# Kernel optimization log

Hardware: AMD Instinct MI355X
Metric: run time of the kernel (lower is better)

## Reference

```python
import jax, jax.numpy as jnp
import numpy as np

B, NB, K, C, CM, POS = 8, 1024, 9, 32, 128, 2
SIGMA = 0.5
NEG_SLOPE = 0.01  # nn.LeakyReLU default
BN_EPS = 1e-5


def _leaky(x):
    return jnp.where(x >= 0, x, NEG_SLOPE * x)


def _batchnorm(x, gamma, beta):
    # BatchNorm1d, training-mode batch statistics over the point dimension
    mu = jnp.mean(x, axis=0)
    var = jnp.mean((x - mu) ** 2, axis=0)
    return gamma * (x - mu) * jax.lax.rsqrt(var + BN_EPS) + beta


def setup_inputs() -> dict:
    key = jax.random.key(0)
    ks = jax.random.split(key, 8)
    N = B * NB
    positions = jax.random.normal(ks[0], (N, POS), jnp.float32)
    weights = jax.random.normal(ks[1], (N, C), jnp.float32)
    batch = jnp.full((B,), NB, dtype=jnp.int32)  # uniform point counts per graph
    # KernelConv params: kernel_init='grid' -> 3x3 grid of offsets spanning +-sigma
    g = jnp.linspace(-SIGMA, SIGMA, 3, dtype=jnp.float32)
    kernel_positions = jnp.stack(jnp.meshgrid(g, g, indexing='ij'), axis=-1).reshape(K, POS)
    kernel_weights = (jax.random.normal(ks[2], (K, C, C), jnp.float32) / np.float32(np.sqrt(C * K)))
    conv_norm_gamma = jnp.ones((C,), jnp.float32)
    conv_norm_beta = jnp.zeros((C,), jnp.float32)
    # PyG MLP([C, CM, C+POS], act_first=True, plain_last=True)
    W1 = jax.random.normal(ks[3], (C, CM), jnp.float32) / np.float32(np.sqrt(C))
    b1 = jnp.zeros((CM,), jnp.float32)
    bn_gamma = jnp.ones((CM,), jnp.float32)
    bn_beta = jnp.zeros((CM,), jnp.float32)
    W2 = jax.random.normal(ks[4], (CM, C + POS), jnp.float32) / np.float32(np.sqrt(CM))
    b2 = jnp.zeros((C + POS,), jnp.float32)
    return dict(positions=positions, weights=weights, batch=batch,
                kernel_positions=kernel_positions, kernel_weights=kernel_weights,
                conv_norm_gamma=conv_norm_gamma, conv_norm_beta=conv_norm_beta,
                W1=W1, b1=b1, bn_gamma=bn_gamma, bn_beta=bn_beta, W2=W2, b2=b2)


def reference(positions, weights, batch, kernel_positions, kernel_weights,
              conv_norm_gamma, conv_norm_beta, W1, b1, bn_gamma, bn_beta, W2, b2):
    N = positions.shape[0]
    # --- KernelConv: each point spawns K components at pos + kernel offset ---
    conv_pos = (positions[:, None, :] + kernel_positions[None, :, :])  # [N,K,2]
    conv_w = jnp.einsum('nc,kcd->nkd', weights, kernel_weights)        # [N,K,C]
    conv_pos = conv_pos.reshape(B, NB * K, POS)
    conv_w = conv_w.reshape(B, NB * K, C)
    # --- KernelSample: evaluate Gaussian mixture at original positions ---
    p = positions.reshape(B, NB, POS)
    d2 = (jnp.sum(p * p, -1)[:, :, None]
          + jnp.sum(conv_pos * conv_pos, -1)[:, None, :]
          - 2.0 * jnp.einsum('bnd,bmd->bnm', p, conv_pos))             # [B,NB,NB*K]
    Kmat = jnp.exp(-d2 / (2.0 * SIGMA * SIGMA))
    sampled = jnp.einsum('bnm,bmc->bnc', Kmat, conv_w).reshape(N, C)
    x = _leaky(sampled)                                                 # KernelSample nonlinearity
    # conv_norm + residual add of input weights
    x = _batchnorm(x, conv_norm_gamma, conv_norm_beta) + weights
    # MLP: lin -> act -> batchnorm (act_first) -> plain last lin
    h = _batchnorm(_leaky(x @ W1 + b1), bn_gamma, bn_beta)
    mlp_out = h @ W2 + b2                                               # [N, POS + C]
    delta_pos, delta_w = mlp_out[:, :POS], mlp_out[:, POS:]
    return positions + delta_pos, x + delta_w
```

## Files before the change

kernel.cpp:

```cpp
#include <hip/hip_runtime.h>
#include <hip/hip_bf16.h>

#define BB    8
#define NBB   1024
#define KK    9
#define CC    32
#define CMM   128
#define NTOT  (BB*NBB)
#define MM    (NBB*KK)
#define MS    16
#define MR    (MM/MS)
#define NEG   0.01f
#define EPS   1e-5f
#define L2C   (-2.8853900817779268f)

#define OFF_CWT   0
#define SZ_CWT    (BB*CC*MM/2)
#define OFF_CFX   (OFF_CWT + SZ_CWT)
#define OFF_CFY   (OFF_CFX + BB*MM)
#define OFF_CF0   (OFF_CFY + BB*MM)
#define OFF_PART  (OFF_CF0 + BB*MM)
#define SZ_ONE    (NTOT*CC)
#define SZ_PART   (MS*SZ_ONE)
#define OFF_X0    (OFF_PART)
#define OFF_X     (OFF_PART + SZ_ONE)
#define OFF_H0    (OFF_PART + 2*SZ_ONE)
#define OFF_ST    (OFF_PART + SZ_PART)

typedef __attribute__((ext_vector_type(8))) short short8;
typedef __attribute__((ext_vector_type(4))) float f32x4;
typedef __attribute__((ext_vector_type(2))) float f32x2;

static __device__ __forceinline__ unsigned short f2bf_rne(float f) {
    __hip_bfloat16 h = __float2bfloat16(f);
    return *reinterpret_cast<unsigned short*>(&h);
}

__global__ __launch_bounds__(256) void k_prep(const float* __restrict__ pos,
                                              const float* __restrict__ kpos,
                                              float* __restrict__ cfx,
                                              float* __restrict__ cfy,
                                              float* __restrict__ cf0,
                                              float* __restrict__ stats) {
    int gid = blockIdx.x*256 + threadIdx.x;
    if (blockIdx.x == 0 && threadIdx.x < 320) stats[threadIdx.x] = 0.f;
    if (gid < BB*MM) {
        int b = gid / MM;
        int m = gid - b*MM;
        int np = m / 9, k9 = m - np*9;
        float qx = pos[((size_t)(b*NBB + np))*2 + 0] + kpos[k9*2 + 0];
        float qy = pos[((size_t)(b*NBB + np))*2 + 1] + kpos[k9*2 + 1];
        cfx[gid] = -2.f*L2C*qx;
        cfy[gid] = -2.f*L2C*qy;
        cf0[gid] = L2C*(qx*qx + qy*qy);
    }
}

__global__ __launch_bounds__(256) void k_convw(const float* __restrict__ w,
                                               const float* __restrict__ kw,
                                               short* __restrict__ cwT) {
    __shared__ unsigned short tile[4*32*144];
    int t = threadIdx.x;
    int l = t & 63, wv = t >> 6;
    int lane15 = l & 15, quad = l >> 4;
    int blk = blockIdx.x;
    int b = blk >> 4, nbl = blk & 15;
    int n = b*NBB + nbl*64 + wv*16 + lane15;

    f32x4 w0 = *(const f32x4*)&w[(size_t)n*CC + quad*8];
    f32x4 w1 = *(const f32x4*)&w[(size_t)n*CC + quad*8 + 4];
    union { unsigned short us[8]; short8 s; } bfr;
    bfr.us[0] = f2bf_rne(w0.x); bfr.us[1] = f2bf_rne(w0.y);
    bfr.us[2] = f2bf_rne(w0.z); bfr.us[3] = f2bf_rne(w0.w);
    bfr.us[4] = f2bf_rne(w1.x); bfr.us[5] = f2bf_rne(w1.y);
    bfr.us[6] = f2bf_rne(w1.z); bfr.us[7] = f2bf_rne(w1.w);

    f32x4 acc[KK][2];
    #pragma unroll
    for (int kk = 0; kk < KK; ++kk) {
        #pragma unroll
        for (int ct = 0; ct < 2; ++ct) {
            int c = ct*16 + lane15;
            union { unsigned short us[8]; short8 s; } afr;
            #pragma unroll
            for (int j = 0; j < 8; ++j)
                afr.us[j] = f2bf_rne(kw[(size_t)(kk*CC + quad*8 + j)*CC + c]);
            acc[kk][ct] = __builtin_amdgcn_mfma_f32_16x16x32_bf16(
                afr.s, bfr.s, (f32x4)0.f, 0, 0, 0);
        }
    }
    unsigned short* tw = tile + wv*4608;
    #pragma unroll
    for (int kk = 0; kk < KK; ++kk)
        #pragma unroll
        for (int ct = 0; ct < 2; ++ct)
            #pragma unroll
            for (int reg = 0; reg < 4; ++reg) {
                int c = ct*16 + quad*4 + reg;
                tw[c*144 + lane15*9 + kk] = f2bf_rne(acc[kk][ct][reg]);
            }
    __syncthreads();
    short* dst = cwT + (size_t)b*CC*MM + (size_t)(nbl*64 + wv*16)*9;
    #pragma unroll
    for (int it = 0; it < 9; ++it) {
        int u = it*64 + l;
        int c = u / 18, seg = u - c*18;
        short8 v = *(const short8*)&tw[c*144 + seg*8];
        *(short8*)&dst[(size_t)c*MM + seg*8] = v;
    }
}

__global__ __launch_bounds__(256) void k_sample(const float* __restrict__ pos,
                                                const float* __restrict__ cfx,
                                                const float* __restrict__ cfy,
                                                const float* __restrict__ cf0,
                                                const short* __restrict__ cwT,
                                                float* __restrict__ part) {
    int t = threadIdx.x;
    int l = t & 63, w = t >> 6;
    int blk = blockIdx.x;
    int ks = blk & 15, nb = (blk >> 4) & 7, b = blk >> 7;
    int lane15 = l & 15, quad = l >> 4;
    int nbase = b*NBB + nb*128 + w*32;

    float px[2], py[2], cn[2];
    #pragma unroll
    for (int nt = 0; nt < 2; ++nt) {
        int n = nbase + nt*16 + lane15;
        float x = pos[(size_t)n*2], y = pos[(size_t)n*2 + 1];
        px[nt] = x; py[nt] = y; cn[nt] = L2C*(x*x + y*y);
    }
    f32x4 acc[2][2];
    #pragma unroll
    for (int nt = 0; nt < 2; ++nt) { acc[nt][0] = (f32x4)0.f; acc[nt][1] = (f32x4)0.f; }

    const float* bx = cfx + (size_t)b*MM;
    const float* by = cfy + (size_t)b*MM;
    const float* b0 = cf0 + (size_t)b*MM;
    const short* ca0 = cwT + (size_t)b*CC*MM + (size_t)lane15*MM;
    const short* ca1 = ca0 + (size_t)16*MM;

    int m0 = ks*MR + quad*8;
    #pragma unroll 2
    for (int kk = 0; kk < MR/32; ++kk, m0 += 32) {
        short8 a0 = *(const short8*)&ca0[m0];
        short8 a1 = *(const short8*)&ca1[m0];
        f32x4 vx0 = *(const f32x4*)&bx[m0];
        f32x4 vx1 = *(const f32x4*)&bx[m0 + 4];
        f32x4 vy0 = *(const f32x4*)&by[m0];
        f32x4 vy1 = *(const f32x4*)&by[m0 + 4];
        f32x4 v00 = *(const f32x4*)&b0[m0];
        f32x4 v01 = *(const f32x4*)&b0[m0 + 4];
        #pragma unroll
        for (int nt = 0; nt < 2; ++nt) {
            f32x2 Xv = {px[nt], px[nt]};
            f32x2 Yv = {py[nt], py[nt]};
            f32x2 Cv = {cn[nt], cn[nt]};
            f32x2 t0 = (f32x2){v00.x, v00.y} + Cv;
            t0 = (f32x2){vy0.x, vy0.y}*Yv + t0;
            t0 = (f32x2){vx0.x, vx0.y}*Xv + t0;
            f32x2 t1 = (f32x2){v00.z, v00.w} + Cv;
            t1 = (f32x2){vy0.z, vy0.w}*Yv + t1;
            t1 = (f32x2){vx0.z, vx0.w}*Xv + t1;
            f32x2 t2 = (f32x2){v01.x, v01.y} + Cv;
            t2 = (f32x2){vy1.x, vy1.y}*Yv + t2;
            t2 = (f32x2){vx1.x, vx1.y}*Xv + t2;
            f32x2 t3 = (f32x2){v01.z, v01.w} + Cv;
            t3 = (f32x2){vy1.z, vy1.w}*Yv + t3;
            t3 = (f32x2){vx1.z, vx1.w}*Xv + t3;
            float e0 = __builtin_amdgcn_exp2f(t0.x);
            float e1 = __builtin_amdgcn_exp2f(t0.y);
            float e2 = __builtin_amdgcn_exp2f(t1.x);
            float e3 = __builtin_amdgcn_exp2f(t1.y);
            float e4 = __builtin_amdgcn_exp2f(t2.x);
            float e5 = __builtin_amdgcn_exp2f(t2.y);
            float e6 = __builtin_amdgcn_exp2f(t3.x);
            float e7 = __builtin_amdgcn_exp2f(t3.y);
            union { unsigned int u[4]; short8 s; } bf;
            bf.u[0] = (__float_as_uint(e0) >> 16) | (__float_as_uint(e1) & 0xffff0000u);
            bf.u[1] = (__float_as_uint(e2) >> 16) | (__float_as_uint(e3) & 0xffff0000u);
            bf.u[2] = (__float_as_uint(e4) >> 16) | (__float_as_uint(e5) & 0xffff0000u);
            bf.u[3] = (__float_as_uint(e6) >> 16) | (__float_as_uint(e7) & 0xffff0000u);
            acc[nt][0] = __builtin_amdgcn_mfma_f32_16x16x32_bf16(a0, bf.s, acc[nt][0], 0, 0, 0);
            acc[nt][1] = __builtin_amdgcn_mfma_f32_16x16x32_bf16(a1, bf.s, acc[nt][1], 0, 0, 0);
        }
    }
    #pragma unroll
    for (int nt = 0; nt < 2; ++nt) {
        int n = nbase + nt*16 + lane15;
        #pragma unroll
        for (int ct = 0; ct < 2; ++ct) {
            int c = ct*16 + quad*4;
            *(f32x4*)&part[((size_t)ks*NTOT + n)*CC + c] = acc[nt][ct];
        }
    }
}

__global__ __launch_bounds__(256) void k_leaky_stats(const float* __restrict__ part,
                                                     float* __restrict__ x0,
                                                     float* __restrict__ s1) {
    __shared__ float ss[32], sq[32];
    int t = threadIdx.x;
    if (t < 32) { ss[t] = 0.f; sq[t] = 0.f; }
    __syncthreads();
    float lsum = 0.f, lsq = 0.f;
    int base = blockIdx.x * 1024;
    for (int j = 0; j < 4; ++j) {
        int idx = base + j*256 + t;
        float v = 0.f;
        #pragma unroll
        for (int s = 0; s < MS; ++s) v += part[(size_t)s*SZ_ONE + idx];
        v = v >= 0.f ? v : NEG*v;
        x0[idx] = v;
        lsum += v; lsq = fmaf(v, v, lsq);
    }
    atomicAdd(&ss[t & 31], lsum);
    atomicAdd(&sq[t & 31], lsq);
    __syncthreads();
    if (t < 32) { atomicAdd(&s1[t], ss[t]); atomicAdd(&s1[32+t], sq[t]); }
}

__global__ __launch_bounds__(256) void k_mlp1(const float* __restrict__ x0,
                                              const float* __restrict__ wts,
                                              const float* __restrict__ gma,
                                              const float* __restrict__ bta,
                                              const float* __restrict__ W1,
                                              const float* __restrict__ b1,
                                              const float* __restrict__ s1,
                                              float* __restrict__ x,
                                              float* __restrict__ h0,
                                              float* __restrict__ s2) {
    __shared__ float tile[64*68];
    int t = threadIdx.x;
    int l = t & 63, w = t >> 6;
    int blk = blockIdx.x;
    int nb = blk >> 1, jh = blk & 1;
    int n = nb*64 + l;
    int j0 = jh*64 + w*16;

    float xv[32];
    #pragma unroll
    for (int c = 0; c < 32; ++c) {
        float mu  = s1[c] * (1.f/NTOT);
        float var = s1[32+c]*(1.f/NTOT) - mu*mu;
        float a   = gma[c] * rsqrtf(var + EPS);
        float v   = x0[(size_t)n*CC + c];
        xv[c] = a*(v - mu) + bta[c] + wts[(size_t)n*CC + c];
    }
    if (jh == 0 && w == 0) {
        #pragma unroll
        for (int c = 0; c < 32; c += 4)
            *(float4*)&x[(size_t)n*CC + c] = make_float4(xv[c], xv[c+1], xv[c+2], xv[c+3]);
    }
    float acc[16];
    #pragma unroll
    for (int jj = 0; jj < 16; ++jj) acc[jj] = b1[j0 + jj];
    #pragma unroll 4
    for (int c = 0; c < 32; ++c) {
        float xc = xv[c];
        const float* w1r = W1 + c*CMM + j0;
        #pragma unroll
        for (int jj = 0; jj < 16; ++jj)
            acc[jj] = fmaf(xc, w1r[jj], acc[jj]);
    }
    float* hd = h0 + (size_t)n*CMM + j0;
    #pragma unroll
    for (int jj = 0; jj < 16; ++jj) {
        acc[jj] = acc[jj] >= 0.f ? acc[jj] : NEG*acc[jj];
        tile[(w*16 + jj)*68 + l] = acc[jj];
    }
    #pragma unroll
    for (int jj = 0; jj < 16; jj += 4)
        *(float4*)&hd[jj] = make_float4(acc[jj], acc[jj+1], acc[jj+2], acc[jj+3]);
    __syncthreads();
    int jl = t >> 2, grp = t & 3;
    float lsum = 0.f, lsq = 0.f;
    #pragma unroll
    for (int q = 0; q < 4; ++q) {
        f32x4 v = *(const f32x4*)&tile[jl*68 + grp*16 + q*4];
        lsum += v.x + v.y + v.z + v.w;
        lsq = fmaf(v.x, v.x, fmaf(v.y, v.y, fmaf(v.z, v.z, fmaf(v.w, v.w, lsq))));
    }
    lsum += __shfl_xor(lsum, 1); lsq += __shfl_xor(lsq, 1);
    lsum += __shfl_xor(lsum, 2); lsq += __shfl_xor(lsq, 2);
    if (grp == 0) {
        int jg = jh*64 + jl;
        atomicAdd(&s2[jg], lsum);
        atomicAdd(&s2[CMM + jg], lsq);
    }
}

__global__ __launch_bounds__(256) void k_mlp2(const float* __restrict__ h0,
                                              const float* __restrict__ x,
                                              const float* __restrict__ pos,
                                              const float* __restrict__ g2,
                                              const float* __restrict__ bt2,
                                              const float* __restrict__ W2,
                                              const float* __restrict__ b2,
                                              const float* __restrict__ s2,
                                              float* __restrict__ out) {
    __shared__ float red[4][64][34];
    int t = threadIdx.x;
    int lane = t & 63, w = t >> 6;
    int n = blockIdx.x*64 + lane;
    int j0 = w*32;
    float hv[32];
    #pragma unroll
    for (int q = 0; q < 8; ++q)
        *(float4*)&hv[q*4] = *(const float4*)&h0[(size_t)n*CMM + j0 + q*4];
    #pragma unroll
    for (int jj = 0; jj < 32; ++jj) {
        int j = j0 + jj;
        float mu  = s2[j] * (1.f/NTOT);
        float var = s2[CMM+j]*(1.f/NTOT) - mu*mu;
        float a   = g2[j] * rsqrtf(var + EPS);
        hv[jj] = a*(hv[jj] - mu) + bt2[j];
    }
    float acc[34];
    #pragma unroll
    for (int c = 0; c < 34; ++c) acc[c] = 0.f;
    for (int jj = 0; jj < 32; ++jj) {
        float h = hv[jj];
        const float* w2r = W2 + (size_t)(j0 + jj)*34;
        #pragma unroll
        for (int c = 0; c < 34; ++c)
            acc[c] = fmaf(h, w2r[c], acc[c]);
    }
    #pragma unroll
    for (int c = 0; c < 34; ++c) red[w][lane][c] = acc[c];
    __syncthreads();
    int r = t & 63, seg = t >> 6;
    int c0 = seg*9, c1 = c0 + 9 < 34 ? c0 + 9 : 34;
    int nn = blockIdx.x*64 + r;
    for (int c = c0; c < c1; ++c) {
        float v = red[0][r][c] + red[1][r][c] + red[2][r][c] + red[3][r][c] + b2[c];
        if (c < 2)
            out[(size_t)nn*2 + c] = pos[(size_t)nn*2 + c] + v;
        else
            out[16384 + (size_t)nn*32 + (c-2)] = x[(size_t)nn*32 + (c-2)] + v;
    }
}

extern "C" void kernel_launch(void* const* d_in, const int* in_sizes, int n_in,
                              void* d_out, int out_size, void* d_ws, size_t ws_size,
                              hipStream_t stream) {
    const float* positions = (const float*)d_in[0];
    const float* weights   = (const float*)d_in[1];
    const float* kpos = (const float*)d_in[3];
    const float* kw   = (const float*)d_in[4];
    const float* cg   = (const float*)d_in[5];
    const float* cb   = (const float*)d_in[6];
    const float* W1   = (const float*)d_in[7];
    const float* b1   = (const float*)d_in[8];
    const float* bg   = (const float*)d_in[9];
    const float* bb   = (const float*)d_in[10];
    const float* W2   = (const float*)d_in[11];
    const float* b2   = (const float*)d_in[12];
    float* ws  = (float*)d_ws;
    float* out = (float*)d_out;

    float* s1 = ws + OFF_ST;
    float* s2 = ws + OFF_ST + 64;

    k_prep<<<288, 256, 0, stream>>>(positions, kpos, ws + OFF_CFX, ws + OFF_CFY,
                                    ws + OFF_CF0, s1);
    k_convw<<<128, 256, 0, stream>>>(weights, kw, (short*)(ws + OFF_CWT));
    k_sample<<<1024, 256, 0, stream>>>(positions, ws + OFF_CFX, ws + OFF_CFY,
                                       ws + OFF_CF0, (const short*)(ws + OFF_CWT),
                                       ws + OFF_PART);
    k_leaky_stats<<<256, 256, 0, stream>>>(ws + OFF_PART, ws + OFF_X0, s1);
    k_mlp1<<<256, 256, 0, stream>>>(ws + OFF_X0, weights, cg, cb, W1, b1,
                                    s1, ws + OFF_X, ws + OFF_H0, s2);
    k_mlp2<<<128, 256, 0, stream>>>(ws + OFF_H0, ws + OFF_X, positions,
                                    bg, bb, W2, b2, s2, out);
}
```

Baseline: 167.4 us.

## Fuse prep into convw, stage kernel weights in LDS, widen mlp2 grid

Merges the conv-position coefficient prep kernel into k_convw, removing one launch. Each block now converts the kernel weights to bf16 and transposes them into shared memory once, replacing the per-lane strided global loads and conversions that fed the MFMA operands. k_mlp2 is split so each block handles 32 points with 8 partial reductions over 16 hidden units, doubling the grid to 256 blocks for more parallelism. The cost is redundant per-block kernel-weight conversion, more shared memory, and a wider cross-partial reduction.

```diff
diff --git a/kernel.cpp b/kernel.cpp
--- a/kernel.cpp
+++ b/kernel.cpp
@@ -36,36 +36,51 @@
     return *reinterpret_cast<unsigned short*>(&h);
 }
 
-__global__ __launch_bounds__(256) void k_prep(const float* __restrict__ pos,
-                                              const float* __restrict__ kpos,
-                                              float* __restrict__ cfx,
-                                              float* __restrict__ cfy,
-                                              float* __restrict__ cf0,
-                                              float* __restrict__ stats) {
-    int gid = blockIdx.x*256 + threadIdx.x;
-    if (blockIdx.x == 0 && threadIdx.x < 320) stats[threadIdx.x] = 0.f;
-    if (gid < BB*MM) {
-        int b = gid / MM;
-        int m = gid - b*MM;
-        int np = m / 9, k9 = m - np*9;
-        float qx = pos[((size_t)(b*NBB + np))*2 + 0] + kpos[k9*2 + 0];
-        float qy = pos[((size_t)(b*NBB + np))*2 + 1] + kpos[k9*2 + 1];
-        cfx[gid] = -2.f*L2C*qx;
-        cfy[gid] = -2.f*L2C*qy;
-        cf0[gid] = L2C*(qx*qx + qy*qy);
-    }
-}
-
-__global__ __launch_bounds__(256) void k_convw(const float* __restrict__ w,
+__global__ __launch_bounds__(256) void k_convw(const float* __restrict__ pos,
+                                               const float* __restrict__ kpos,
+                                               const float* __restrict__ w,
                                                const float* __restrict__ kw,
+                                               float* __restrict__ cfx,
+                                               float* __restrict__ cfy,
+                                               float* __restrict__ cf0,
+                                               float* __restrict__ stats,
                                                short* __restrict__ cwT) {
     __shared__ unsigned short tile[4*32*144];
+    __shared__ unsigned short kwl[KK*CC*CC];
     int t = threadIdx.x;
     int l = t & 63, wv = t >> 6;
     int lane15 = l & 15, quad = l >> 4;
     int blk = blockIdx.x;
     int b = blk >> 4, nbl = blk & 15;
     int n = b*NBB + nbl*64 + wv*16 + lane15;
+
+    if (blk == 0 && t < 320) stats[t] = 0.f;
+    #pragma unroll
+    for (int rep = 0; rep < 3; ++rep) {
+        int gid = blk*256 + t + rep*32768;
+        if (gid < BB*MM) {
+            int bb = gid / MM;
+            int m = gid - bb*MM;
+            int np = m / 9, k9 = m - np*9;
+            float qx = pos[((size_t)(bb*NBB + np))*2 + 0] + kpos[k9*2 + 0];
+            float qy = pos[((size_t)(bb*NBB + np))*2 + 1] + kpos[k9*2 + 1];
+            cfx[gid] = -2.f*L2C*qx;
+            cfy[gid] = -2.f*L2C*qy;
+            cf0[gid] = L2C*(qx*qx + qy*qy);
+        }
+    }
+
+    for (int u = t; u < KK*CC*CC/4; u += 256) {
+        int flat = u*4;
+        int row  = flat >> 5;
+        int c0   = flat & 31;
+        int kk = row >> 5, cp = row & 31;
+        f32x4 v = *(const f32x4*)&kw[flat];
+        kwl[(kk*CC + c0+0)*CC + cp] = f2bf_rne(v.x);
+        kwl[(kk*CC + c0+1)*CC + cp] = f2bf_rne(v.y);
+        kwl[(kk*CC + c0+2)*CC + cp] = f2bf_rne(v.z);
+        kwl[(kk*CC + c0+3)*CC + cp] = f2bf_rne(v.w);
+    }
 
     f32x4 w0 = *(const f32x4*)&w[(size_t)n*CC + quad*8];
     f32x4 w1 = *(const f32x4*)&w[(size_t)n*CC + quad*8 + 4];
@@ -75,18 +90,17 @@
     bfr.us[4] = f2bf_rne(w1.x); bfr.us[5] = f2bf_rne(w1.y);
     bfr.us[6] = f2bf_rne(w1.z); bfr.us[7] = f2bf_rne(w1.w);
 
+    __syncthreads();
+
     f32x4 acc[KK][2];
     #pragma unroll
     for (int kk = 0; kk < KK; ++kk) {
         #pragma unroll
         for (int ct = 0; ct < 2; ++ct) {
             int c = ct*16 + lane15;
-            union { unsigned short us[8]; short8 s; } afr;
-            #pragma unroll
-            for (int j = 0; j < 8; ++j)
-                afr.us[j] = f2bf_rne(kw[(size_t)(kk*CC + quad*8 + j)*CC + c]);
+            short8 afr = *(const short8*)&kwl[(kk*CC + c)*CC + quad*8];
             acc[kk][ct] = __builtin_amdgcn_mfma_f32_16x16x32_bf16(
-                afr.s, bfr.s, (f32x4)0.f, 0, 0, 0);
+                afr, bfr.s, (f32x4)0.f, 0, 0, 0);
         }
     }
     unsigned short* tw = tile + wv*4608;
@@ -299,17 +313,19 @@
                                               const float* __restrict__ b2,
                                               const float* __restrict__ s2,
                                               float* __restrict__ out) {
-    __shared__ float red[4][64][34];
+    __shared__ float red[8][32][35];
     int t = threadIdx.x;
     int lane = t & 63, w = t >> 6;
-    int n = blockIdx.x*64 + lane;
-    int j0 = w*32;
-    float hv[32];
-    #pragma unroll
-    for (int q = 0; q < 8; ++q)
+    int half = lane >> 5;
+    int nl = lane & 31;
+    int n = blockIdx.x*32 + nl;
+    int j0 = w*32 + half*16;
+    float hv[16];
+    #pragma unroll
+    for (int q = 0; q < 4; ++q)
         *(float4*)&hv[q*4] = *(const float4*)&h0[(size_t)n*CMM + j0 + q*4];
     #pragma unroll
-    for (int jj = 0; jj < 32; ++jj) {
+    for (int jj = 0; jj < 16; ++jj) {
         int j = j0 + jj;
         float mu  = s2[j] * (1.f/NTOT);
         float var = s2[CMM+j]*(1.f/NTOT) - mu*mu;
@@ -319,21 +335,22 @@
     float acc[34];
     #pragma unroll
     for (int c = 0; c < 34; ++c) acc[c] = 0.f;
-    for (int jj = 0; jj < 32; ++jj) {
+    for (int jj = 0; jj < 16; ++jj) {
         float h = hv[jj];
         const float* w2r = W2 + (size_t)(j0 + jj)*34;
         #pragma unroll
         for (int c = 0; c < 34; ++c)
             acc[c] = fmaf(h, w2r[c], acc[c]);
     }
-    #pragma unroll
-    for (int c = 0; c < 34; ++c) red[w][lane][c] = acc[c];
-    __syncthreads();
-    int r = t & 63, seg = t >> 6;
-    int c0 = seg*9, c1 = c0 + 9 < 34 ? c0 + 9 : 34;
-    int nn = blockIdx.x*64 + r;
-    for (int c = c0; c < c1; ++c) {
-        float v = red[0][r][c] + red[1][r][c] + red[2][r][c] + red[3][r][c] + b2[c];
+    int rid = w*2 + half;
+    #pragma unroll
+    for (int c = 0; c < 34; ++c) red[rid][nl][c] = acc[c];
+    __syncthreads();
+    for (int u = t; u < 32*34; u += 256) {
+        int r = u / 34, c = u - r*34;
+        float v = red[0][r][c] + red[1][r][c] + red[2][r][c] + red[3][r][c]
+                + red[4][r][c] + red[5][r][c] + red[6][r][c] + red[7][r][c] + b2[c];
+        int nn = blockIdx.x*32 + r;
         if (c < 2)
             out[(size_t)nn*2 + c] = pos[(size_t)nn*2 + c] + v;
         else
@@ -362,15 +379,15 @@
     float* s1 = ws + OFF_ST;
     float* s2 = ws + OFF_ST + 64;
 
-    k_prep<<<288, 256, 0, stream>>>(positions, kpos, ws + OFF_CFX, ws + OFF_CFY,
-                                    ws + OFF_CF0, s1);
-    k_convw<<<128, 256, 0, stream>>>(weights, kw, (short*)(ws + OFF_CWT));
+    k_convw<<<128, 256, 0, stream>>>(positions, kpos, weights, kw,
+                                     ws + OFF_CFX, ws + OFF_CFY, ws + OFF_CF0,
+                                     s1, (short*)(ws + OFF_CWT));
     k_sample<<<1024, 256, 0, stream>>>(positions, ws + OFF_CFX, ws + OFF_CFY,
                                        ws + OFF_CF0, (const short*)(ws + OFF_CWT),
                                        ws + OFF_PART);
     k_leaky_stats<<<256, 256, 0, stream>>>(ws + OFF_PART, ws + OFF_X0, s1);
     k_mlp1<<<256, 256, 0, stream>>>(ws + OFF_X0, weights, cg, cb, W1, b1,
                                     s1, ws + OFF_X, ws + OFF_H0, s2);
-    k_mlp2<<<128, 256, 0, stream>>>(ws + OFF_H0, ws + OFF_X, positions,
+    k_mlp2<<<256, 256, 0, stream>>>(ws + OFF_H0, ws + OFF_X, positions,
                                     bg, bb, W2, b2, s2, out);
 }
```

New measurement: 159.2 us. 4.9% less time.
